# Performance work log

Measured on AMD Instinct MI355X. Metric: run time of the kernel, lower is better.

Reference implementation:

```python
import jax, jax.numpy as jnp
import numpy as np

E = 512          # embed_dim
H = 8            # num_heads
FF = 2048        # ff_dim
MAX_LEN = 5000   # DynamicPositionalEncoding max_len
LN_EPS = 1e-5


def _layernorm(x, g, b):
    mu = jnp.mean(x, axis=-1, keepdims=True)
    var = jnp.mean((x - mu) ** 2, axis=-1, keepdims=True)
    return (x - mu) / jnp.sqrt(var + LN_EPS) * g + b


def setup_inputs() -> dict:
    key = jax.random.key(0)
    ks = jax.random.split(key, 12)
    S, B = 2048, 4
    s = 0.02
    return {
        "x": jax.random.normal(ks[0], (S, B, E), dtype=jnp.float32),
        "pos": jnp.zeros((1, MAX_LEN, E), dtype=jnp.float32),  # torch init: zeros Parameter
        "in_proj_w": jax.random.normal(ks[1], (3 * E, E), dtype=jnp.float32) * s,
        "in_proj_b": jnp.zeros((3 * E,), dtype=jnp.float32),
        "out_w": jax.random.normal(ks[2], (E, E), dtype=jnp.float32) * s,
        "out_b": jnp.zeros((E,), dtype=jnp.float32),
        "w1": jax.random.normal(ks[3], (FF, E), dtype=jnp.float32) * s,
        "b1": jnp.zeros((FF,), dtype=jnp.float32),
        "w2": jax.random.normal(ks[4], (E, FF), dtype=jnp.float32) * s,
        "b2": jnp.zeros((E,), dtype=jnp.float32),
        "g1": jnp.ones((E,), dtype=jnp.float32),
        "be1": jnp.zeros((E,), dtype=jnp.float32),
        "g2": jnp.ones((E,), dtype=jnp.float32),
        "be2": jnp.zeros((E,), dtype=jnp.float32),
        "local_window_size": 128,
    }


def reference(x, pos, in_proj_w, in_proj_b, out_w, out_b, w1, b1, w2, b2,
              g1, be1, g2, be2, local_window_size):
    S, B, _ = x.shape
    w = int(local_window_size)
    # quirk of original: pos encoding sliced by x.size(1) == batch, broadcast over seq
    x = x + pos[:, :B, :]

    # additive mask: local window [i-w, i+w] allowed, plus global columns every 2w
    i = jnp.arange(S)[:, None]
    j = jnp.arange(S)[None, :]
    allowed = (jnp.abs(i - j) <= w) | (j % (2 * w) == 0)
    mask = jnp.where(allowed, 0.0, -jnp.inf).astype(x.dtype)  # (S, S)

    # multihead self-attention (torch MHA semantics, seq-first)
    qkv = x @ in_proj_w.T + in_proj_b                 # (S, B, 3E)
    q, k, v = jnp.split(qkv, 3, axis=-1)
    hd = E // H

    def heads(t):  # (S, B, E) -> (B, H, S, hd)
        return t.reshape(S, B, H, hd).transpose(1, 2, 0, 3)

    q, k, v = heads(q), heads(k), heads(v)
    scale = 1.0 / jnp.sqrt(jnp.asarray(hd, x.dtype))
    scores = jnp.einsum("bhqd,bhkd->bhqk", q * scale, k) + mask
    attn = jax.nn.softmax(scores, axis=-1)
    y = jnp.einsum("bhqk,bhkd->bhqd", attn, v)        # (B, H, S, hd)
    y = y.transpose(2, 0, 1, 3).reshape(S, B, E)
    attn_out = y @ out_w.T + out_b

    x = _layernorm(x + attn_out, g1, be1)
    ff = jax.nn.relu(x @ w1.T + b1) @ w2.T + b2
    x = _layernorm(x + ff, g2, be2)
    return x
```

## Files before the change

### kernel.cpp

```cpp
#include <hip/hip_runtime.h>
#include <hip/hip_bf16.h>
#include <math.h>

#define S_LEN 2048
#define B_SZ  4
#define E_DIM 512
#define H_NUM 8
#define HD    64
#define FF_DIM 2048
#define NROWS 8192
#define WIN   128

typedef unsigned short u16;
typedef __bf16 bf16x8 __attribute__((ext_vector_type(8)));
typedef float  f32x4  __attribute__((ext_vector_type(4)));

__device__ __forceinline__ u16 f2bf(float f) {
  union { float f; unsigned u; } v; v.f = f;
  unsigned u = v.u;
  return (u16)((u + 0x7fffu + ((u >> 16) & 1u)) >> 16);
}

__device__ __forceinline__ void gl_lds16(const u16* gp, u16* lp) {
  __builtin_amdgcn_global_load_lds(
      (const __attribute__((address_space(1))) unsigned int*)gp,
      (__attribute__((address_space(3))) unsigned int*)lp, 16, 0, 0);
}

__global__ __launch_bounds__(256) void wcast_kernel(
    const float* __restrict__ s0, const float* __restrict__ s1,
    const float* __restrict__ s2, const float* __restrict__ s3,
    u16* __restrict__ d0, u16* __restrict__ d1,
    u16* __restrict__ d2, u16* __restrict__ d3) {
  const int n0 = 196608, n1 = 65536, n2 = 262144;
  int i = blockIdx.x * blockDim.x + threadIdx.x;
  const float4* sp; ushort4* dp; int off;
  if (i < n0)                { sp = (const float4*)s0; dp = (ushort4*)d0; off = i; }
  else if (i < n0 + n1)      { sp = (const float4*)s1; dp = (ushort4*)d1; off = i - n0; }
  else if (i < n0 + n1 + n2) { sp = (const float4*)s2; dp = (ushort4*)d2; off = i - n0 - n1; }
  else                       { sp = (const float4*)s3; dp = (ushort4*)d3; off = i - n0 - n1 - n2; }
  float4 v = sp[off];
  ushort4 o; o.x = f2bf(v.x); o.y = f2bf(v.y); o.z = f2bf(v.z); o.w = f2bf(v.w);
  dp[off] = o;
}

__global__ __launch_bounds__(256) void add_pos_kernel(
    const float* __restrict__ x, const float* __restrict__ pos,
    float* __restrict__ xp, u16* __restrict__ xpb) {
  int idx = blockIdx.x * blockDim.x + threadIdx.x;
  float4 xv = ((const float4*)x)[idx];
  float4 pv = ((const float4*)pos)[idx & 511];
  float4 o;
  o.x = xv.x + pv.x; o.y = xv.y + pv.y; o.z = xv.z + pv.z; o.w = xv.w + pv.w;
  ((float4*)xp)[idx] = o;
  ushort4 ob; ob.x = f2bf(o.x); ob.y = f2bf(o.y); ob.z = f2bf(o.z); ob.w = f2bf(o.w);
  ((ushort4*)xpb)[idx] = ob;
}

#define GBK 64

template <int BN, int GY>
__global__ __launch_bounds__(256) void mfma_gemm(
    const u16* __restrict__ A, const u16* __restrict__ W,
    const float* __restrict__ bias, float* __restrict__ outf,
    u16* __restrict__ outb, int M, int N, int K, int mode,
    u16* __restrict__ qb, u16* __restrict__ kb, u16* __restrict__ vb) {
  constexpr int TJ = BN / 32;
  __shared__ u16 SMEM[2 * 128 * GBK + 2 * BN * GBK];
  u16* As0 = SMEM;
  u16* Bs0 = SMEM + 2 * 128 * GBK;
  int tid = threadIdx.x;
  int lane = tid & 63;
  int w = tid >> 6;
  int lin = blockIdx.y * 64 + blockIdx.x;
  int xcd = lin & 7, slot = lin >> 3;
  int jj = slot % GY;
  int mm = (slot / GY) * 8 + xcd;
  int m0 = mm * 128;
  int j0 = jj * BN;
  int wrow = (w >> 1) * 64;
  int wcol = (w & 1) * (BN / 2);
  int lm = lane & 15;
  int kq = lane >> 4;
  int sw = lm & 7;
  int r8 = lane >> 3;
  int csrc = ((lane & 7) ^ r8) << 3;

  f32x4 acc[4][TJ];
#pragma unroll
  for (int i = 0; i < 4; i++)
#pragma unroll
    for (int j = 0; j < TJ; j++) acc[i][j] = (f32x4){0.f, 0.f, 0.f, 0.f};

  const u16* Ab = A + (size_t)m0 * K;
  const u16* Wb = W + (size_t)j0 * K;

  size_t soff[4];
#pragma unroll
  for (int u = 0; u < 4; u++)
    soff[u] = (size_t)(u * 32 + w * 8 + r8) * K + csrc;

  auto stage = [&](int kt, int pb) {
#pragma unroll
    for (int u = 0; u < 4; u++)
      gl_lds16(&Ab[soff[u] + kt], &As0[pb * 128 * GBK + (u * 4 + w) * 512]);
#pragma unroll
    for (int u = 0; u < TJ; u++)
      gl_lds16(&Wb[soff[u] + kt], &Bs0[pb * BN * GBK + (u * 4 + w) * 512]);
  };

  stage(0, 0);
  int pb = 0;
  for (int kt = 0; kt < K; kt += GBK) {
    __syncthreads();
    if (kt + GBK < K) stage(kt + GBK, pb ^ 1);
#pragma unroll
    for (int k2 = 0; k2 < GBK; k2 += 32) {
      int cc = ((((k2 >> 3) + kq) ^ sw) << 3);
      bf16x8 af[4], bfr[TJ];
#pragma unroll
      for (int t = 0; t < 4; t++)
        af[t] = *(const bf16x8*)&As0[pb * 128 * GBK + (wrow + t * 16 + lm) * GBK + cc];
#pragma unroll
      for (int tj = 0; tj < TJ; tj++)
        bfr[tj] = *(const bf16x8*)&Bs0[pb * BN * GBK + (wcol + tj * 16 + lm) * GBK + cc];
#pragma unroll
      for (int ti = 0; ti < 4; ti++)
#pragma unroll
        for (int tj = 0; tj < TJ; tj++)
          acc[ti][tj] = __builtin_amdgcn_mfma_f32_16x16x32_bf16(
              af[ti], bfr[tj], acc[ti][tj], 0, 0, 0);
    }
    pb ^= 1;
  }

  __syncthreads();
  if (mode == 0) {
    float* Cf = (float*)SMEM;
    constexpr int CF = BN + 4;
#pragma unroll
    for (int p = 0; p < 2; p++) {
      if ((w >> 1) == p) {
#pragma unroll
        for (int tj = 0; tj < TJ; tj++) {
          float bv = bias[j0 + wcol + tj * 16 + lm];
#pragma unroll
          for (int ti = 0; ti < 4; ti++)
#pragma unroll
            for (int r = 0; r < 4; r++)
              Cf[(ti * 16 + kq * 4 + r) * CF + wcol + tj * 16 + lm] =
                  acc[ti][tj][r] + bv;
        }
      }
      __syncthreads();
      constexpr int RC4 = BN / 4;
#pragma unroll
      for (int it = 0; it < 64 * RC4 / 256; it++) {
        int id = it * 256 + tid;
        int row = id / RC4, c4 = (id % RC4) * 4;
        float4 vq = *(float4*)&Cf[row * CF + c4];
        *(float4*)&outf[(size_t)(m0 + p * 64 + row) * N + j0 + c4] = vq;
      }
      __syncthreads();
    }
  } else {
    u16* Cs = (u16*)SMEM;
    constexpr int CS = BN + 8;
    int which = j0 >> 9;
    float qsc = (mode == 2 && which == 0) ? 0.125f : 1.f;
#pragma unroll
    for (int tj = 0; tj < TJ; tj++) {
      float bv = bias[j0 + wcol + tj * 16 + lm];
#pragma unroll
      for (int ti = 0; ti < 4; ti++)
#pragma unroll
        for (int r = 0; r < 4; r++) {
          float val = acc[ti][tj][r] + bv;
          if (mode == 1) val = fmaxf(val, 0.f);
          Cs[(wrow + ti * 16 + kq * 4 + r) * CS + wcol + tj * 16 + lm] =
              f2bf(val * qsc);
        }
    }
    __syncthreads();
    constexpr int RC8 = BN / 8;
#pragma unroll
    for (int it = 0; it < 128 * RC8 / 256; it++) {
      int id = it * 256 + tid;
      int row = id / RC8, c8 = (id % RC8) * 8;
      uint4 vq = *(uint4*)&Cs[row * CS + c8];
      if (mode == 1) {
        *(uint4*)&outb[(size_t)(m0 + row) * N + j0 + c8] = vq;
      } else {
        int e = (j0 & 511) + c8;
        int h = e >> 6, d0 = e & 63;
        int m = m0 + row, s = m >> 2, b = m & 3;
        u16* dst = (which == 0) ? qb : (which == 1) ? kb : vb;
        *(uint4*)&dst[((size_t)(b * H_NUM + h) * S_LEN + s) * HD + d0] = vq;
      }
    }
  }
}

#define PST 72

__global__ __launch_bounds__(256) void attn_mfma_kernel(
    const u16* __restrict__ q, const u16* __restrict__ k,
    const u16* __restrict__ v, u16* __restrict__ yb) {
  __shared__ u16 Qs[64 * 64];
  __shared__ u16 Ks[64 * 64];
  __shared__ u16 Vs[64 * 64];
  __shared__ u16 Ps[64 * PST];
  int tid = threadIdx.x, lane = tid & 63, w = tid >> 6;
  int quad = lane >> 4, lm = lane & 15;
  int sw = lm & 7;
  int r8 = lane >> 3;
  int csrc = ((lane & 7) ^ r8) << 3;
  int lin = blockIdx.y * 32 + blockIdx.x;
  int xcd = lin & 7, slot = lin >> 3;
  int bh = xcd * 4 + (slot >> 5);
  int i0 = (slot & 31) * 64;
  int b = bh >> 3, h = bh & 7;
  const u16* qp = q + ((size_t)bh * S_LEN + i0) * HD;
  const u16* kp = k + (size_t)bh * S_LEN * HD;
  const u16* vp = v + (size_t)bh * S_LEN * HD;

#pragma unroll
  for (int u = 0; u < 2; u++) {
    int seg = u * 4 + w;
    int r = seg * 8 + r8;
    gl_lds16(&qp[(size_t)r * HD + csrc], &Qs[seg * 512]);
  }

  int cl = i0 - WIN; if (cl < 0) cl = 0;
  int chi = i0 + 63 + WIN; if (chi > S_LEN - 1) chi = S_LEN - 1;
  int nch = (chi - cl + 64) >> 6;
  int tlo = (cl + 255) >> 8;
  int thi0 = (chi >> 8) + 1;
  int ng = tlo + 8 - thi0;

  float m_i[4], l_i[4];
  f32x4 o[4];
#pragma unroll
  for (int r = 0; r < 4; r++) { m_i[r] = -INFINITY; l_i[r] = 0.f; }
#pragma unroll
  for (int tj = 0; tj < 4; tj++) o[tj] = (f32x4){0.f, 0.f, 0.f, 0.f};

  for (int ch = 0; ch <= nch; ch++) {
    bool is_g = (ch == nch);
    int c0 = cl + (ch << 6);
    __syncthreads();
    if (!is_g) {
#pragma unroll
      for (int u = 0; u < 2; u++) {
        int seg = u * 4 + w;
        int r = seg * 8 + r8;
        gl_lds16(&kp[(size_t)(c0 + r) * HD + csrc], &Ks[seg * 512]);
      }
#pragma unroll
      for (int it = 0; it < 4; it++) {
        int flat = it * 256 + tid;
        int c = flat >> 4;
        int d0 = (flat & 15) << 2;
        ushort4 vv = make_ushort4(0, 0, 0, 0);
        int src = c0 + c;
        if (src <= chi) vv = *(const ushort4*)&vp[(size_t)src * HD + d0];
        u16 arr[4] = {vv.x, vv.y, vv.z, vv.w};
#pragma unroll
        for (int jd = 0; jd < 4; jd++) {
          int d = d0 + jd;
          Vs[d * 64 + ((((c >> 3) ^ (d & 7)) << 3) | (c & 7))] = arr[jd];
        }
      }
    } else {
      if (w == 0) {
        int rr = lane >> 3;
        int grow = (rr < tlo) ? (rr << 8) : ((thi0 + rr - tlo) << 8);
        if (rr >= ng) grow = 0;
        gl_lds16(&kp[(size_t)grow * HD + (((lane & 7) ^ rr) << 3)], &Ks[0]);
      }
      for (int e = tid; e < 64 * 8; e += 256) {
        int d = e & 63, cg = e >> 6;
        if (cg < ng) {
          int gs = (cg < tlo) ? (cg << 8) : ((thi0 + cg - tlo) << 8);
          Vs[d * 64 + ((d & 7) << 3) + cg] = vp[(size_t)gs * HD + d];
        }
      }
    }
    __syncthreads();

    f32x4 s[4];
#pragma unroll
    for (int tj = 0; tj < 4; tj++) s[tj] = (f32x4){0.f, 0.f, 0.f, 0.f};
#pragma unroll
    for (int k2 = 0; k2 < 64; k2 += 32) {
      int cb = (k2 >> 3) + quad;
      bf16x8 a = *(const bf16x8*)&Qs[(w * 16 + lm) * 64 + ((cb ^ sw) << 3)];
#pragma unroll
      for (int tj = 0; tj < 4; tj++) {
        bf16x8 bfr = *(const bf16x8*)&Ks[(tj * 16 + lm) * 64 + ((cb ^ sw) << 3)];
        s[tj] = __builtin_amdgcn_mfma_f32_16x16x32_bf16(a, bfr, s[tj], 0, 0, 0);
      }
    }
#pragma unroll
    for (int tj = 0; tj < 4; tj++) {
      int cidx = tj * 16 + lm;
      bool inval = is_g ? (cidx >= ng) : (c0 + cidx > chi);
      if (inval) {
        s[tj][0] = -INFINITY; s[tj][1] = -INFINITY;
        s[tj][2] = -INFINITY; s[tj][3] = -INFINITY;
      }
    }
#pragma unroll
    for (int r = 0; r < 4; r++) {
      float mx = fmaxf(fmaxf(s[0][r], s[1][r]), fmaxf(s[2][r], s[3][r]));
      mx = fmaxf(mx, __shfl_xor(mx, 1)); mx = fmaxf(mx, __shfl_xor(mx, 2));
      mx = fmaxf(mx, __shfl_xor(mx, 4)); mx = fmaxf(mx, __shfl_xor(mx, 8));
      float mnew = fmaxf(m_i[r], mx);
      float al = __expf(m_i[r] - mnew);
      float rs = 0.f;
#pragma unroll
      for (int tj = 0; tj < 4; tj++) {
        float p = __expf(s[tj][r] - mnew);
        s[tj][r] = p; rs += p;
      }
      rs += __shfl_xor(rs, 1); rs += __shfl_xor(rs, 2);
      rs += __shfl_xor(rs, 4); rs += __shfl_xor(rs, 8);
      l_i[r] = l_i[r] * al + rs;
      m_i[r] = mnew;
      o[0][r] *= al; o[1][r] *= al; o[2][r] *= al; o[3][r] *= al;
    }
#pragma unroll
    for (int tj = 0; tj < 4; tj++)
#pragma unroll
      for (int r = 0; r < 4; r++)
        Ps[(w * 16 + quad * 4 + r) * PST + tj * 16 + lm] = f2bf(s[tj][r]);
#pragma unroll
    for (int k2 = 0; k2 < 64; k2 += 32) {
      int cb = (k2 >> 3) + quad;
      bf16x8 a = *(const bf16x8*)&Ps[(w * 16 + lm) * PST + k2 + quad * 8];
#pragma unroll
      for (int tj = 0; tj < 4; tj++) {
        bf16x8 bfr = *(const bf16x8*)&Vs[(tj * 16 + lm) * 64 + ((cb ^ sw) << 3)];
        o[tj] = __builtin_amdgcn_mfma_f32_16x16x32_bf16(a, bfr, o[tj], 0, 0, 0);
      }
    }
  }

  __syncthreads();
#pragma unroll
  for (int r = 0; r < 4; r++) {
    float inv = 1.f / l_i[r];
#pragma unroll
    for (int tj = 0; tj < 4; tj++)
      Qs[(w * 16 + quad * 4 + r) * 64 + tj * 16 + lm] = f2bf(o[tj][r] * inv);
  }
  __syncthreads();
#pragma unroll
  for (int it = 0; it < 2; it++) {
    int id = it * 256 + tid;
    int row = id >> 3, c8 = (id & 7) * 8;
    uint4 vq = *(uint4*)&Qs[row * 64 + c8];
    *(uint4*)&yb[((size_t)(i0 + row) * B_SZ + b) * E_DIM + h * HD + c8] = vq;
  }
}

__global__ __launch_bounds__(256) void add_ln_kernel(
    const float* __restrict__ a, const float* __restrict__ r,
    const float* __restrict__ g, const float* __restrict__ be,
    float* __restrict__ out, u16* __restrict__ outb) {
  int wave = threadIdx.x >> 6;
  int lane = threadIdx.x & 63;
  int row = blockIdx.x * 4 + wave;
  const float* ar = a + (size_t)row * E_DIM;
  const float* rr = r + (size_t)row * E_DIM;
  float vals[8];
  float s = 0.f;
#pragma unroll
  for (int t = 0; t < 8; t++) {
    vals[t] = ar[t * 64 + lane] + rr[t * 64 + lane];
    s += vals[t];
  }
#pragma unroll
  for (int o = 32; o >= 1; o >>= 1) s += __shfl_xor(s, o, 64);
  float mu = s * (1.f / E_DIM);
  float vs = 0.f;
#pragma unroll
  for (int t = 0; t < 8; t++) { float d = vals[t] - mu; vs += d * d; }
#pragma unroll
  for (int o = 32; o >= 1; o >>= 1) vs += __shfl_xor(vs, o, 64);
  float inv = rsqrtf(vs * (1.f / E_DIM) + 1e-5f);
  float* orow = out + (size_t)row * E_DIM;
  u16* obrow = outb ? outb + (size_t)row * E_DIM : nullptr;
#pragma unroll
  for (int t = 0; t < 8; t++) {
    int e = t * 64 + lane;
    float val = (vals[t] - mu) * inv * g[e] + be[e];
    orow[e] = val;
    if (obrow) obrow[e] = f2bf(val);
  }
}

extern "C" void kernel_launch(void* const* d_in, const int* in_sizes, int n_in,
                              void* d_out, int out_size, void* d_ws, size_t ws_size,
                              hipStream_t stream) {
  const float* x     = (const float*)d_in[0];
  const float* pos   = (const float*)d_in[1];
  const float* in_w  = (const float*)d_in[2];
  const float* in_b  = (const float*)d_in[3];
  const float* out_w = (const float*)d_in[4];
  const float* out_b = (const float*)d_in[5];
  const float* w1    = (const float*)d_in[6];
  const float* b1    = (const float*)d_in[7];
  const float* w2    = (const float*)d_in[8];
  const float* b2    = (const float*)d_in[9];
  const float* g1    = (const float*)d_in[10];
  const float* be1   = (const float*)d_in[11];
  const float* g2    = (const float*)d_in[12];
  const float* be2   = (const float*)d_in[13];
  float* out = (float*)d_out;

  char* base = (char*)d_ws;
  float* xp    = (float*)(base);
  u16*   xpb   = (u16*)(base + ((size_t)16 << 20));
  u16*   qb    = (u16*)(base + ((size_t)24 << 20));
  u16*   kb    = (u16*)(base + ((size_t)32 << 20));
  u16*   vb    = (u16*)(base + ((size_t)40 << 20));
  u16*   ybf   = (u16*)(base + ((size_t)48 << 20));
  float* aprj  = (float*)(base + ((size_t)56 << 20));
  u16*   inwb  = (u16*)(base + ((size_t)72 << 20));
  u16*   outwb = (u16*)(base + ((size_t)74 << 20));
  u16*   w1b   = (u16*)(base + ((size_t)76 << 20));
  u16*   w2b   = (u16*)(base + ((size_t)78 << 20));
  float* x1    = xp;
  u16*   x1b   = xpb;
  u16*   ff1b  = qb;
  float* ff2   = aprj;

  wcast_kernel<<<3072, 256, 0, stream>>>(in_w, out_w, w1, w2, inwb, outwb, w1b, w2b);
  add_pos_kernel<<<4096, 256, 0, stream>>>(x, pos, xp, xpb);
  mfma_gemm<128, 12><<<dim3(64, 12), 256, 0, stream>>>(xpb, inwb, in_b, nullptr, nullptr,
                                                       NROWS, 1536, 512, 2, qb, kb, vb);
  attn_mfma_kernel<<<dim3(32, 32), 256, 0, stream>>>(qb, kb, vb, ybf);
  mfma_gemm<64, 8><<<dim3(64, 8), 256, 0, stream>>>(ybf, outwb, out_b, aprj, nullptr,
                                                    NROWS, 512, 512, 0, nullptr, nullptr, nullptr);
  add_ln_kernel<<<2048, 256, 0, stream>>>(xp, aprj, g1, be1, x1, x1b);
  mfma_gemm<128, 16><<<dim3(64, 16), 256, 0, stream>>>(x1b, w1b, b1, nullptr, ff1b,
                                                       NROWS, 2048, 512, 1, nullptr, nullptr, nullptr);
  mfma_gemm<64, 8><<<dim3(64, 8), 256, 0, stream>>>(ff1b, w2b, b2, ff2, nullptr,
                                                    NROWS, 512, 2048, 0, nullptr, nullptr, nullptr);
  add_ln_kernel<<<2048, 256, 0, stream>>>(x1, ff2, g2, be2, out, nullptr);
}
```

Baseline: 249.5 us.

## Pre-transpose V and double-buffer K/V staging in local-window attention

Adds a separate kernel that transposes V into a head-major, d-by-sequence layout. The attention kernel can then load V tiles with async global-to-LDS copies instead of scalar transposing stores. K/V tiles are double-buffered so the next chunk's loads are issued while the current chunk computes, which also removes one barrier per iteration. Q fragments are kept in registers, and the P buffer uses an XOR swizzle rather than padding. The cost is an extra kernel launch plus a full V read/write pass.

```diff
diff --git a/kernel.cpp b/kernel.cpp
--- a/kernel.cpp
+++ b/kernel.cpp
@@ -201,15 +201,43 @@
   }
 }
 
-#define PST 72
+__global__ __launch_bounds__(256) void vtrans_kernel(
+    const u16* __restrict__ vb, u16* __restrict__ vt) {
+  __shared__ u16 T[64 * 72];
+  int tid = threadIdx.x;
+  int bh = blockIdx.y, sc = blockIdx.x;
+  const u16* src = vb + ((size_t)bh * S_LEN + sc * 64) * HD;
+#pragma unroll
+  for (int it = 0; it < 2; it++) {
+    int id = it * 256 + tid;
+    int srow = id >> 3, d8 = (id & 7) * 8;
+    ushort4 v0 = *(const ushort4*)&src[srow * HD + d8];
+    ushort4 v1 = *(const ushort4*)&src[srow * HD + d8 + 4];
+    u16 arr[8] = {v0.x, v0.y, v0.z, v0.w, v1.x, v1.y, v1.z, v1.w};
+#pragma unroll
+    for (int j = 0; j < 8; j++) {
+      int d = d8 + j;
+      int rs = srow ^ (((d >> 3) & 7) << 3);
+      T[d * 72 + rs] = arr[j];
+    }
+  }
+  __syncthreads();
+#pragma unroll
+  for (int it = 0; it < 2; it++) {
+    int id = it * 256 + tid;
+    int d = id >> 3, s8 = (id & 7) * 8;
+    int blk = (s8 >> 3) ^ ((d >> 3) & 7);
+    uint4 vq = *(uint4*)&T[d * 72 + (blk << 3)];
+    *(uint4*)&vt[((size_t)bh * HD + d) * S_LEN + sc * 64 + s8] = vq;
+  }
+}
 
 __global__ __launch_bounds__(256) void attn_mfma_kernel(
     const u16* __restrict__ q, const u16* __restrict__ k,
-    const u16* __restrict__ v, u16* __restrict__ yb) {
-  __shared__ u16 Qs[64 * 64];
-  __shared__ u16 Ks[64 * 64];
-  __shared__ u16 Vs[64 * 64];
-  __shared__ u16 Ps[64 * PST];
+    const u16* __restrict__ vt, u16* __restrict__ yb) {
+  __shared__ u16 Ks[2 * 4096];
+  __shared__ u16 Vs[2 * 4096];
+  __shared__ u16 Ps[4096];
   int tid = threadIdx.x, lane = tid & 63, w = tid >> 6;
   int quad = lane >> 4, lm = lane & 15;
   int sw = lm & 7;
@@ -222,13 +250,13 @@
   int b = bh >> 3, h = bh & 7;
   const u16* qp = q + ((size_t)bh * S_LEN + i0) * HD;
   const u16* kp = k + (size_t)bh * S_LEN * HD;
-  const u16* vp = v + (size_t)bh * S_LEN * HD;
-
-#pragma unroll
-  for (int u = 0; u < 2; u++) {
-    int seg = u * 4 + w;
-    int r = seg * 8 + r8;
-    gl_lds16(&qp[(size_t)r * HD + csrc], &Qs[seg * 512]);
+  const u16* vp = vt + (size_t)bh * HD * S_LEN;
+
+  bf16x8 qreg[2];
+  {
+    const u16* qr = qp + (size_t)(w * 16 + lm) * HD + quad * 8;
+    qreg[0] = *(const bf16x8*)&qr[0];
+    qreg[1] = *(const bf16x8*)&qr[32];
   }
 
   int cl = i0 - WIN; if (cl < 0) cl = 0;
@@ -238,6 +266,32 @@
   int thi0 = (chi >> 8) + 1;
   int ng = tlo + 8 - thi0;
 
+  auto stage_local = [&](int ch, int pbuf) {
+    int c0 = cl + (ch << 6);
+#pragma unroll
+    for (int u = 0; u < 2; u++) {
+      int seg = u * 4 + w;
+      int r = seg * 8 + r8;
+      gl_lds16(&kp[(size_t)(c0 + r) * HD + csrc], &Ks[pbuf * 4096 + seg * 512]);
+      gl_lds16(&vp[(size_t)r * S_LEN + c0 + csrc], &Vs[pbuf * 4096 + seg * 512]);
+    }
+  };
+  auto stage_global = [&](int pbuf) {
+    if (w == 0) {
+      int rr = lane >> 3;
+      int grow = (rr < tlo) ? (rr << 8) : ((thi0 + rr - tlo) << 8);
+      if (rr >= ng) grow = 0;
+      gl_lds16(&kp[(size_t)grow * HD + (((lane & 7) ^ rr) << 3)], &Ks[pbuf * 4096]);
+    }
+    for (int e = tid; e < 64 * 8; e += 256) {
+      int d = e & 63, cg = e >> 6;
+      if (cg < ng) {
+        int gs = (cg < tlo) ? (cg << 8) : ((thi0 + cg - tlo) << 8);
+        Vs[pbuf * 4096 + d * 64 + ((d & 7) << 3) + cg] = vp[(size_t)d * S_LEN + gs];
+      }
+    }
+  };
+
   float m_i[4], l_i[4];
   f32x4 o[4];
 #pragma unroll
@@ -245,48 +299,16 @@
 #pragma unroll
   for (int tj = 0; tj < 4; tj++) o[tj] = (f32x4){0.f, 0.f, 0.f, 0.f};
 
+  stage_local(0, 0);
+  __syncthreads();
+  int pb = 0;
   for (int ch = 0; ch <= nch; ch++) {
     bool is_g = (ch == nch);
     int c0 = cl + (ch << 6);
-    __syncthreads();
-    if (!is_g) {
-#pragma unroll
-      for (int u = 0; u < 2; u++) {
-        int seg = u * 4 + w;
-        int r = seg * 8 + r8;
-        gl_lds16(&kp[(size_t)(c0 + r) * HD + csrc], &Ks[seg * 512]);
-      }
-#pragma unroll
-      for (int it = 0; it < 4; it++) {
-        int flat = it * 256 + tid;
-        int c = flat >> 4;
-        int d0 = (flat & 15) << 2;
-        ushort4 vv = make_ushort4(0, 0, 0, 0);
-        int src = c0 + c;
-        if (src <= chi) vv = *(const ushort4*)&vp[(size_t)src * HD + d0];
-        u16 arr[4] = {vv.x, vv.y, vv.z, vv.w};
-#pragma unroll
-        for (int jd = 0; jd < 4; jd++) {
-          int d = d0 + jd;
-          Vs[d * 64 + ((((c >> 3) ^ (d & 7)) << 3) | (c & 7))] = arr[jd];
-        }
-      }
-    } else {
-      if (w == 0) {
-        int rr = lane >> 3;
-        int grow = (rr < tlo) ? (rr << 8) : ((thi0 + rr - tlo) << 8);
-        if (rr >= ng) grow = 0;
-        gl_lds16(&kp[(size_t)grow * HD + (((lane & 7) ^ rr) << 3)], &Ks[0]);
-      }
-      for (int e = tid; e < 64 * 8; e += 256) {
-        int d = e & 63, cg = e >> 6;
-        if (cg < ng) {
-          int gs = (cg < tlo) ? (cg << 8) : ((thi0 + cg - tlo) << 8);
-          Vs[d * 64 + ((d & 7) << 3) + cg] = vp[(size_t)gs * HD + d];
-        }
-      }
-    }
-    __syncthreads();
+    if (ch < nch) {
+      if (ch + 1 < nch) stage_local(ch + 1, pb ^ 1);
+      else stage_global(pb ^ 1);
+    }
 
     f32x4 s[4];
 #pragma unroll
@@ -294,10 +316,10 @@
 #pragma unroll
     for (int k2 = 0; k2 < 64; k2 += 32) {
       int cb = (k2 >> 3) + quad;
-      bf16x8 a = *(const bf16x8*)&Qs[(w * 16 + lm) * 64 + ((cb ^ sw) << 3)];
+      bf16x8 a = qreg[k2 >> 5];
 #pragma unroll
       for (int tj = 0; tj < 4; tj++) {
-        bf16x8 bfr = *(const bf16x8*)&Ks[(tj * 16 + lm) * 64 + ((cb ^ sw) << 3)];
+        bf16x8 bfr = *(const bf16x8*)&Ks[pb * 4096 + (tj * 16 + lm) * 64 + ((cb ^ sw) << 3)];
         s[tj] = __builtin_amdgcn_mfma_f32_16x16x32_bf16(a, bfr, s[tj], 0, 0, 0);
       }
     }
@@ -332,34 +354,43 @@
 #pragma unroll
     for (int tj = 0; tj < 4; tj++)
 #pragma unroll
-      for (int r = 0; r < 4; r++)
-        Ps[(w * 16 + quad * 4 + r) * PST + tj * 16 + lm] = f2bf(s[tj][r]);
+      for (int r = 0; r < 4; r++) {
+        int rowp = w * 16 + quad * 4 + r;
+        int blk = (tj * 2 + (lm >> 3)) ^ (rowp & 7);
+        Ps[rowp * 64 + (blk << 3) + (lm & 7)] = f2bf(s[tj][r]);
+      }
 #pragma unroll
     for (int k2 = 0; k2 < 64; k2 += 32) {
       int cb = (k2 >> 3) + quad;
-      bf16x8 a = *(const bf16x8*)&Ps[(w * 16 + lm) * PST + k2 + quad * 8];
+      int blkr = cb ^ sw;
+      bf16x8 a = *(const bf16x8*)&Ps[(w * 16 + lm) * 64 + (blkr << 3)];
 #pragma unroll
       for (int tj = 0; tj < 4; tj++) {
-        bf16x8 bfr = *(const bf16x8*)&Vs[(tj * 16 + lm) * 64 + ((cb ^ sw) << 3)];
+        bf16x8 bfr = *(const bf16x8*)&Vs[pb * 4096 + (tj * 16 + lm) * 64 + ((cb ^ sw) << 3)];
         o[tj] = __builtin_amdgcn_mfma_f32_16x16x32_bf16(a, bfr, o[tj], 0, 0, 0);
       }
     }
-  }
-
-  __syncthreads();
+    __syncthreads();
+    pb ^= 1;
+  }
+
 #pragma unroll
   for (int r = 0; r < 4; r++) {
     float inv = 1.f / l_i[r];
 #pragma unroll
-    for (int tj = 0; tj < 4; tj++)
-      Qs[(w * 16 + quad * 4 + r) * 64 + tj * 16 + lm] = f2bf(o[tj][r] * inv);
+    for (int tj = 0; tj < 4; tj++) {
+      int rowp = w * 16 + quad * 4 + r;
+      int blk = (tj * 2 + (lm >> 3)) ^ (rowp & 7);
+      Ps[rowp * 64 + (blk << 3) + (lm & 7)] = f2bf(o[tj][r] * inv);
+    }
   }
   __syncthreads();
 #pragma unroll
   for (int it = 0; it < 2; it++) {
     int id = it * 256 + tid;
     int row = id >> 3, c8 = (id & 7) * 8;
-    uint4 vq = *(uint4*)&Qs[row * 64 + c8];
+    int blk = (id & 7) ^ (row & 7);
+    uint4 vq = *(uint4*)&Ps[row * 64 + (blk << 3)];
     *(uint4*)&yb[((size_t)(i0 + row) * B_SZ + b) * E_DIM + h * HD + c8] = vq;
   }
 }
@@ -427,6 +458,7 @@
   u16*   vb    = (u16*)(base + ((size_t)40 << 20));
   u16*   ybf   = (u16*)(base + ((size_t)48 << 20));
   float* aprj  = (float*)(base + ((size_t)56 << 20));
+  u16*   vt    = (u16*)(base + ((size_t)56 << 20));
   u16*   inwb  = (u16*)(base + ((size_t)72 << 20));
   u16*   outwb = (u16*)(base + ((size_t)74 << 20));
   u16*   w1b   = (u16*)(base + ((size_t)76 << 20));
@@ -440,7 +472,8 @@
   add_pos_kernel<<<4096, 256, 0, stream>>>(x, pos, xp, xpb);
   mfma_gemm<128, 12><<<dim3(64, 12), 256, 0, stream>>>(xpb, inwb, in_b, nullptr, nullptr,
                                                        NROWS, 1536, 512, 2, qb, kb, vb);
-  attn_mfma_kernel<<<dim3(32, 32), 256, 0, stream>>>(qb, kb, vb, ybf);
+  vtrans_kernel<<<dim3(32, 32), 256, 0, stream>>>(vb, vt);
+  attn_mfma_kernel<<<dim3(32, 32), 256, 0, stream>>>(qb, kb, vt, ybf);
   mfma_gemm<64, 8><<<dim3(64, 8), 256, 0, stream>>>(ybf, outwb, out_b, aprj, nullptr,
                                                     NROWS, 512, 512, 0, nullptr, nullptr, nullptr);
   add_ln_kernel<<<2048, 256, 0, stream>>>(xp, aprj, g1, be1, x1, x1b);
```

Result: no change. 246.4 us (-1.3%).
